# Kernel optimization log

Measured on AMD Instinct MI355X. Metric: run time of the kernel, lower is better.

The kernel has to match this reference:

```python
import jax, jax.numpy as jnp
import numpy as np

DIM, DK, DV = 1024, 128, 128

def setup_inputs() -> dict:
    key = jax.random.key(0)
    ks = jax.random.split(key, 7)
    X = jax.random.normal(ks[0], (4, 4096, DIM), dtype=jnp.float32)
    s = DIM ** -0.5
    Wq = jax.random.normal(ks[1], (DIM, DK), dtype=jnp.float32) * s
    bq = jnp.zeros((DK,), dtype=jnp.float32)
    Wk = jax.random.normal(ks[2], (DIM, DK), dtype=jnp.float32) * s
    bk = jnp.zeros((DK,), dtype=jnp.float32)
    Wv = jax.random.normal(ks[3], (DIM, DV), dtype=jnp.float32) * s
    bv = jnp.zeros((DV,), dtype=jnp.float32)
    return {"X": X, "Wq": Wq, "bq": bq, "Wk": Wk, "bk": bk, "Wv": Wv, "bv": bv}

def reference(X, Wq, bq, Wk, bk, Wv, bv):
    scale = DK ** -0.5
    q = X @ Wq + bq              # [B, S, dk]
    k = X @ Wk + bk              # [B, S, dk]
    v = X @ Wv + bv              # [B, S, dv]
    attn = jnp.einsum('bqd,bkd->bqk', q, k) * scale  # [B, S, S]
    attn = jax.nn.softmax(attn, axis=-1)
    return jnp.einsum('bqk,bkd->bqd', attn, v)       # [B, S, dv]
```

## Files before the change

### kernel.cpp

```cpp
#include <hip/hip_runtime.h>

#define NB 4
#define SEQ 4096
#define DIMK 1024
#define DKV 128
#define SCALE 0.08838834764831845f

typedef float  f32x4  __attribute__((ext_vector_type(4)));
typedef float  f32x16 __attribute__((ext_vector_type(16)));
typedef _Float16 f16x8 __attribute__((ext_vector_type(8)));

static __device__ __forceinline__ int pkrtz(float a, float b) {
    auto h = __builtin_amdgcn_cvt_pkrtz(a, b);
    return __builtin_bit_cast(int, h);
}

__global__ void prep_wt(const float* __restrict__ Wq, const float* __restrict__ Wk,
                        const float* __restrict__ Wv, _Float16* __restrict__ WT) {
    int tid = blockIdx.x * 256 + threadIdx.x;
    int n  = tid & 127;
    int k  = (tid >> 7) & 1023;
    int w3 = tid >> 17;
    const float* W = (w3 == 0) ? Wq : (w3 == 1) ? Wk : Wv;
    WT[((size_t)w3 * 128 + n) * 1024 + k] = (_Float16)W[(size_t)k * 128 + n];
}

__global__ __launch_bounds__(256, 2) void qkv_proj(
    const float* __restrict__ X,
    const float* __restrict__ bq, const float* __restrict__ bk, const float* __restrict__ bv,
    const _Float16* __restrict__ WT,
    _Float16* __restrict__ Qh, _Float16* __restrict__ Kh, _Float16* __restrict__ VTh) {

    __shared__ __attribute__((aligned(16))) char WTs[2][128 * 144];
    const int t = threadIdx.x;
    const int w = t >> 6, l = t & 63;
    const int lrow = l & 15, lg = l >> 4;
    const int w3   = blockIdx.x % 3;
    const int tile = blockIdx.x / 3;
    const int r0 = tile * 64;

    f32x4 acc[8] = {};
    const float* xrow = X + (size_t)(r0 + w * 16 + lrow) * DIMK;
    const _Float16* Wbase = WT + (size_t)w3 * 128 * 1024;

    const int srow = t >> 3, spart = t & 7;

    {
        int4 wreg[4];
        #pragma unroll
        for (int i = 0; i < 4; ++i)
            wreg[i] = *(const int4*)(Wbase + (size_t)(srow + 32 * i) * 1024 + spart * 8);
        #pragma unroll
        for (int i = 0; i < 4; ++i)
            *(int4*)(WTs[0] + (srow + 32 * i) * 144 + spart * 16) = wreg[i];
    }
    float4 xc0 = *(const float4*)(xrow + lg * 8);
    float4 xc1 = *(const float4*)(xrow + lg * 8 + 4);
    float4 xc2 = *(const float4*)(xrow + 32 + lg * 8);
    float4 xc3 = *(const float4*)(xrow + 32 + lg * 8 + 4);
    __syncthreads();

    for (int kt = 0; kt < 16; ++kt) {
        const int cur = kt & 1;
        const int k0n = ((kt + 1) & 15) * 64;
        float4 xn0 = *(const float4*)(xrow + k0n + lg * 8);
        float4 xn1 = *(const float4*)(xrow + k0n + lg * 8 + 4);
        float4 xn2 = *(const float4*)(xrow + k0n + 32 + lg * 8);
        float4 xn3 = *(const float4*)(xrow + k0n + 32 + lg * 8 + 4);
        int4 wreg[4];
        #pragma unroll
        for (int i = 0; i < 4; ++i)
            wreg[i] = *(const int4*)(Wbase + (size_t)(srow + 32 * i) * 1024 + k0n + spart * 8);

        #pragma unroll
        for (int kk = 0; kk < 2; ++kk) {
            f16x8 a;
            float4 u = kk ? xc2 : xc0, v = kk ? xc3 : xc1;
            a[0] = (_Float16)u.x; a[1] = (_Float16)u.y; a[2] = (_Float16)u.z; a[3] = (_Float16)u.w;
            a[4] = (_Float16)v.x; a[5] = (_Float16)v.y; a[6] = (_Float16)v.z; a[7] = (_Float16)v.w;
            #pragma unroll
            for (int n = 0; n < 8; ++n) {
                f16x8 bf = *(const f16x8*)(WTs[cur] + (n * 16 + lrow) * 144 +
                                           kk * 64 + lg * 16);
                acc[n] = __builtin_amdgcn_mfma_f32_16x16x32_f16(a, bf, acc[n], 0, 0, 0);
            }
        }
        #pragma unroll
        for (int i = 0; i < 4; ++i)
            *(int4*)(WTs[cur ^ 1] + (srow + 32 * i) * 144 + spart * 16) = wreg[i];
        __syncthreads();
        xc0 = xn0; xc1 = xn1; xc2 = xn2; xc3 = xn3;
    }

    const float* bias = (w3 == 0) ? bq : (w3 == 1) ? bk : bv;
    #pragma unroll
    for (int n = 0; n < 8; ++n) {
        int col = n * 16 + lrow;
        float bv_ = bias[col];
        #pragma unroll
        for (int j = 0; j < 4; ++j) {
            int grow = r0 + w * 16 + lg * 4 + j;
            float val = acc[n][j] + bv_;
            if (w3 == 0) {
                Qh[(size_t)grow * DKV + col] = (_Float16)(val * SCALE);
            } else if (w3 == 1) {
                Kh[(size_t)grow * DKV + col] = (_Float16)val;
            } else {
                int b = grow >> 12, sp = grow & 4095;
                VTh[((size_t)b * DKV + col) * SEQ + sp] = (_Float16)val;
            }
        }
    }
}

__global__ __launch_bounds__(256, 2) void attn_kernel(
    const _Float16* __restrict__ Qh, const _Float16* __restrict__ Kh,
    const _Float16* __restrict__ VTh, float* __restrict__ out) {

    __shared__ __attribute__((aligned(16))) char lds[65536];

    const int t = threadIdx.x;
    const int w = t >> 6, l = t & 63;
    const int lq = l & 31;
    const int hi = l >> 5;

    const int work = (blockIdx.x & 7) * 64 + (blockIdx.x >> 3);
    const int b  = work >> 7;
    const int qt = work & 127;
    const int q0 = qt * 32;

    char* Kw = lds + w * 16384;
    char* Vw = Kw + 8192;

    f16x8 qf[8];
    #pragma unroll
    for (int c = 0; c < 8; ++c)
        qf[c] = *(const f16x8*)(Qh + (size_t)(b * SEQ + q0 + lq) * DKV + c * 16 + hi * 8);

    f32x16 o[4] = {};
    float m = -INFINITY, lsum = 0.f;

    const _Float16* Kbase = Kh + (size_t)(b * SEQ + w * 1024) * DKV;
    const _Float16* Vbase = VTh + (size_t)b * DKV * SEQ + w * 1024;

    const int krow = l >> 4, kpart = l & 15;
    const int vdv  = l >> 2, vp = l & 3;

    {
        int4 kreg[8], vreg[8];
        #pragma unroll
        for (int i = 0; i < 8; ++i)
            kreg[i] = *(const int4*)(Kbase + (size_t)(krow + 4 * i) * DKV + kpart * 8);
        #pragma unroll
        for (int i = 0; i < 8; ++i)
            vreg[i] = *(const int4*)(Vbase + (size_t)(vdv + 16 * i) * SEQ + vp * 8);
        #pragma unroll
        for (int i = 0; i < 8; ++i) {
            int row = krow + 4 * i;
            *(int4*)(Kw + row * 256 + ((kpart * 16) ^ ((row & 15) << 4))) = kreg[i];
        }
        #pragma unroll
        for (int i = 0; i < 8; ++i) {
            int dv = vdv + 16 * i;
            *(int4*)(Vw + dv * 64 + ((vp ^ ((dv >> 1) & 3)) * 16)) = vreg[i];
        }
    }

    for (int kt = 0; kt < 32; ++kt) {
        const int kn = ((kt + 1) & 31) * 32;
        int4 kreg[8], vreg[8];
        #pragma unroll
        for (int i = 0; i < 8; ++i)
            kreg[i] = *(const int4*)(Kbase + (size_t)(kn + krow + 4 * i) * DKV + kpart * 8);
        #pragma unroll
        for (int i = 0; i < 8; ++i)
            vreg[i] = *(const int4*)(Vbase + (size_t)(vdv + 16 * i) * SEQ + kn + vp * 8);

        asm volatile("s_waitcnt lgkmcnt(0)" ::: "memory");
        __builtin_amdgcn_sched_barrier(0);

        f32x16 sa = {}, sb = {};
        #pragma unroll
        for (int c = 0; c < 4; ++c) {
            f16x8 kfa = *(const f16x8*)(Kw + lq * 256 +
                                        (((2 * c + hi) * 16) ^ ((lq & 15) << 4)));
            f16x8 kfb = *(const f16x8*)(Kw + lq * 256 +
                                        (((2 * (c + 4) + hi) * 16) ^ ((lq & 15) << 4)));
            sa = __builtin_amdgcn_mfma_f32_32x32x16_f16(kfa, qf[c], sa, 0, 0, 0);
            sb = __builtin_amdgcn_mfma_f32_32x32x16_f16(kfb, qf[c + 4], sb, 0, 0, 0);
        }
        f32x16 s = sa + sb;

        float red[8];
        #pragma unroll
        for (int r = 0; r < 8; ++r) red[r] = fmaxf(s[2 * r], s[2 * r + 1]);
        #pragma unroll
        for (int r = 0; r < 4; ++r) red[r] = fmaxf(red[r], red[r + 4]);
        red[0] = fmaxf(red[0], red[2]);
        red[1] = fmaxf(red[1], red[3]);
        float tm = fmaxf(red[0], red[1]);
        tm = fmaxf(tm, __shfl_xor(tm, 32));

        if (__any(tm > m + 8.f)) {
            float mnew = fmaxf(m, tm);
            float corr = __expf(m - mnew);
            m = mnew;
            lsum *= corr;
            #pragma unroll
            for (int dvt = 0; dvt < 4; ++dvt) o[dvt] *= corr;
        }
        #pragma unroll
        for (int r = 0; r < 16; ++r) s[r] = __expf(s[r] - m);
        float sr[8];
        #pragma unroll
        for (int r = 0; r < 8; ++r) sr[r] = s[2 * r] + s[2 * r + 1];
        #pragma unroll
        for (int r = 0; r < 4; ++r) sr[r] += sr[r + 4];
        sr[0] += sr[2]; sr[1] += sr[3];
        float ts = sr[0] + sr[1];
        ts += __shfl_xor(ts, 32);
        lsum += ts;

        int wv[8];
        #pragma unroll
        for (int i = 0; i < 8; ++i) wv[i] = pkrtz(s[2 * i], s[2 * i + 1]);

        #pragma unroll
        for (int s_ = 0; s_ < 2; ++s_) {
            const int base = s_ * 4;
            int x0 = __shfl_xor(wv[base + 0], 32);
            int x1 = __shfl_xor(wv[base + 1], 32);
            int x2 = __shfl_xor(wv[base + 2], 32);
            int x3 = __shfl_xor(wv[base + 3], 32);
            union { int i[4]; f16x8 v; } bu;
            bu.i[0] = hi ? x2 : wv[base + 0];
            bu.i[1] = hi ? x3 : wv[base + 1];
            bu.i[2] = hi ? wv[base + 2] : x0;
            bu.i[3] = hi ? wv[base + 3] : x1;
            #pragma unroll
            for (int dvt = 0; dvt < 4; ++dvt) {
                int rv = dvt * 32 + lq;
                f16x8 vf = *(const f16x8*)(Vw + rv * 64 +
                                           (((s_ * 2 + hi) ^ ((rv >> 1) & 3)) * 16));
                o[dvt] = __builtin_amdgcn_mfma_f32_32x32x16_f16(vf, bu.v, o[dvt], 0, 0, 0);
            }
        }

        #pragma unroll
        for (int i = 0; i < 8; ++i) {
            int row = krow + 4 * i;
            *(int4*)(Kw + row * 256 + ((kpart * 16) ^ ((row & 15) << 4))) = kreg[i];
        }
        #pragma unroll
        for (int i = 0; i < 8; ++i) {
            int dv = vdv + 16 * i;
            *(int4*)(Vw + dv * 64 + ((vp ^ ((dv >> 1) & 3)) * 16)) = vreg[i];
        }
    }

    float* obuf  = (float*)lds;
    float* mlbuf = (float*)(lds + 49152);

    __syncthreads();
    if (w == 1 || w == 3) {
        int sb_ = (w == 3);
        #pragma unroll
        for (int dvt = 0; dvt < 4; ++dvt)
            #pragma unroll
            for (int r = 0; r < 16; ++r)
                obuf[sb_ * 4096 + (dvt * 16 + r) * 64 + l] = o[dvt][r];
        if (l < 32) {
            mlbuf[sb_ * 64 + l * 2 + 0] = m;
            mlbuf[sb_ * 64 + l * 2 + 1] = lsum;
        }
    }
    __syncthreads();
    if (w == 0 || w == 2) {
        int sb_ = (w == 2);
        float mo  = mlbuf[sb_ * 64 + lq * 2 + 0];
        float lo_ = mlbuf[sb_ * 64 + lq * 2 + 1];
        float mn = fmaxf(m, mo);
        float ca = __expf(m - mn);
        float cb = __expf(mo - mn);
        m = mn;
        lsum = lsum * ca + lo_ * cb;
        #pragma unroll
        for (int dvt = 0; dvt < 4; ++dvt)
            #pragma unroll
            for (int r = 0; r < 16; ++r)
                o[dvt][r] = o[dvt][r] * ca + obuf[sb_ * 4096 + (dvt * 16 + r) * 64 + l] * cb;
    }
    __syncthreads();
    if (w == 2) {
        #pragma unroll
        for (int dvt = 0; dvt < 4; ++dvt)
            #pragma unroll
            for (int r = 0; r < 16; ++r)
                obuf[(dvt * 16 + r) * 64 + l] = o[dvt][r];
        if (l < 32) {
            mlbuf[l * 2 + 0] = m;
            mlbuf[l * 2 + 1] = lsum;
        }
    }
    __syncthreads();
    if (w == 0) {
        float mo  = mlbuf[lq * 2 + 0];
        float lo_ = mlbuf[lq * 2 + 1];
        float mn = fmaxf(m, mo);
        float ca = __expf(m - mn);
        float cb = __expf(mo - mn);
        float rl = 1.0f / (lsum * ca + lo_ * cb);
        #pragma unroll
        for (int dvt = 0; dvt < 4; ++dvt)
            #pragma unroll
            for (int r = 0; r < 16; ++r)
                o[dvt][r] = (o[dvt][r] * ca + obuf[(dvt * 16 + r) * 64 + l] * cb) * rl;
    }
    __syncthreads();
    float* tbuf = (float*)lds;
    if (w == 0) {
        #pragma unroll
        for (int dvt = 0; dvt < 4; ++dvt)
            #pragma unroll
            for (int r = 0; r < 16; ++r) {
                int dv = dvt * 32 + (r & 3) + 8 * (r >> 2) + 4 * hi;
                tbuf[lq * 132 + dv] = o[dvt][r];
            }
    }
    __syncthreads();
    const size_t obase = (size_t)(b * SEQ + qt * 32) * DKV;
    int row = t >> 3, c0 = (t & 7) * 16;
    #pragma unroll
    for (int i = 0; i < 4; ++i) {
        float4 v = *(const float4*)(tbuf + row * 132 + c0 + i * 4);
        *(float4*)(out + obase + row * 128 + c0 + i * 4) = v;
    }
}

extern "C" void kernel_launch(void* const* d_in, const int* in_sizes, int n_in,
                              void* d_out, int out_size, void* d_ws, size_t ws_size,
                              hipStream_t stream) {
    const float* X  = (const float*)d_in[0];
    const float* Wq = (const float*)d_in[1];
    const float* bq = (const float*)d_in[2];
    const float* Wk = (const float*)d_in[3];
    const float* bk = (const float*)d_in[4];
    const float* Wv = (const float*)d_in[5];
    const float* bv = (const float*)d_in[6];
    float* out = (float*)d_out;

    const size_t nqe = (size_t)NB * SEQ * DKV;
    _Float16* Qh  = (_Float16*)d_ws;
    _Float16* Kh  = Qh  + nqe;
    _Float16* VTh = Kh  + nqe;
    _Float16* WTh = VTh + nqe;

    prep_wt<<<(3 * 1024 * 128) / 256, 256, 0, stream>>>(Wq, Wk, Wv, WTh);
    qkv_proj<<<(NB * SEQ / 64) * 3, 256, 0, stream>>>(X, bq, bk, bv, WTh, Qh, Kh, VTh);
    attn_kernel<<<NB * 128, 256, 0, stream>>>(Qh, Kh, VTh, out);
}
```

Before: 119.9 us.

## Stage K/V tiles with direct global-to-LDS loads instead of register staging

Replaces the register-staged prefetch of K and V tiles (global load into VGPRs, then LDS store) with global_load_lds 16-byte transfers that write straight into LDS, with the swizzle moved to the global source address. K for the next tile is issued right after the QK MFMAs and V after the PV MFMAs, each guarded by an lgkmcnt wait. This frees the 16 int4 prefetch registers and removes the LDS store instructions. The trade-off is less latency hiding, since the next tile now loads into the same single buffer mid-iteration and the loop waits on vmcnt(0) at the top of every iteration.

```diff
diff --git a/kernel.cpp b/kernel.cpp
--- a/kernel.cpp
+++ b/kernel.cpp
@@ -13,6 +13,11 @@
 static __device__ __forceinline__ int pkrtz(float a, float b) {
     auto h = __builtin_amdgcn_cvt_pkrtz(a, b);
     return __builtin_bit_cast(int, h);
+}
+
+static __device__ __forceinline__ void gll16(const void* g, void* l) {
+    __builtin_amdgcn_global_load_lds((const __attribute__((address_space(1))) char*)g,
+                                     (__attribute__((address_space(3))) char*)l, 16, 0, 0);
 }
 
 __global__ void prep_wt(const float* __restrict__ Wq, const float* __restrict__ Wk,
@@ -143,40 +148,33 @@
     const _Float16* Kbase = Kh + (size_t)(b * SEQ + w * 1024) * DKV;
     const _Float16* Vbase = VTh + (size_t)b * DKV * SEQ + w * 1024;
 
-    const int krow = l >> 4, kpart = l & 15;
-    const int vdv  = l >> 2, vp = l & 3;
-
-    {
-        int4 kreg[8], vreg[8];
-        #pragma unroll
-        for (int i = 0; i < 8; ++i)
-            kreg[i] = *(const int4*)(Kbase + (size_t)(krow + 4 * i) * DKV + kpart * 8);
-        #pragma unroll
-        for (int i = 0; i < 8; ++i)
-            vreg[i] = *(const int4*)(Vbase + (size_t)(vdv + 16 * i) * SEQ + vp * 8);
-        #pragma unroll
-        for (int i = 0; i < 8; ++i) {
-            int row = krow + 4 * i;
-            *(int4*)(Kw + row * 256 + ((kpart * 16) ^ ((row & 15) << 4))) = kreg[i];
-        }
-        #pragma unroll
-        for (int i = 0; i < 8; ++i) {
-            int dv = vdv + 16 * i;
-            *(int4*)(Vw + dv * 64 + ((vp ^ ((dv >> 1) & 3)) * 16)) = vreg[i];
-        }
-    }
+    const int krow_ = l >> 4;
+    const int vdv_  = l >> 2;
+
+#define STAGE_K(KOFF) {                                                                   \
+        _Pragma("unroll")                                                                 \
+        for (int i = 0; i < 8; ++i) {                                                     \
+            int row = 4 * i + krow_;                                                      \
+            int part = (l & 15) ^ (row & 15);                                             \
+            gll16(Kbase + (size_t)((KOFF) + row) * DKV + part * 8, Kw + i * 1024);        \
+        }                                                                                 \
+    }
+#define STAGE_V(KOFF) {                                                                   \
+        _Pragma("unroll")                                                                 \
+        for (int i = 0; i < 8; ++i) {                                                     \
+            int dv = 16 * i + vdv_;                                                       \
+            int p = (l & 3) ^ ((dv >> 1) & 3);                                            \
+            gll16(Vbase + (size_t)dv * SEQ + (KOFF) + p * 8, Vw + i * 1024);              \
+        }                                                                                 \
+    }
+
+    STAGE_K(0)
+    STAGE_V(0)
 
     for (int kt = 0; kt < 32; ++kt) {
         const int kn = ((kt + 1) & 31) * 32;
-        int4 kreg[8], vreg[8];
-        #pragma unroll
-        for (int i = 0; i < 8; ++i)
-            kreg[i] = *(const int4*)(Kbase + (size_t)(kn + krow + 4 * i) * DKV + kpart * 8);
-        #pragma unroll
-        for (int i = 0; i < 8; ++i)
-            vreg[i] = *(const int4*)(Vbase + (size_t)(vdv + 16 * i) * SEQ + kn + vp * 8);
-
-        asm volatile("s_waitcnt lgkmcnt(0)" ::: "memory");
+
+        asm volatile("s_waitcnt vmcnt(0)" ::: "memory");
         __builtin_amdgcn_sched_barrier(0);
 
         f32x16 sa = {}, sb = {};
@@ -190,6 +188,10 @@
             sb = __builtin_amdgcn_mfma_f32_32x32x16_f16(kfb, qf[c + 4], sb, 0, 0, 0);
         }
         f32x16 s = sa + sb;
+
+        asm volatile("s_waitcnt lgkmcnt(0)" ::: "memory");
+        __builtin_amdgcn_sched_barrier(0);
+        STAGE_K(kn)
 
         float red[8];
         #pragma unroll
@@ -246,17 +248,12 @@
             }
         }
 
-        #pragma unroll
-        for (int i = 0; i < 8; ++i) {
-            int row = krow + 4 * i;
-            *(int4*)(Kw + row * 256 + ((kpart * 16) ^ ((row & 15) << 4))) = kreg[i];
-        }
-        #pragma unroll
-        for (int i = 0; i < 8; ++i) {
-            int dv = vdv + 16 * i;
-            *(int4*)(Vw + dv * 64 + ((vp ^ ((dv >> 1) & 3)) * 16)) = vreg[i];
-        }
-    }
+        asm volatile("s_waitcnt lgkmcnt(0)" ::: "memory");
+        __builtin_amdgcn_sched_barrier(0);
+        STAGE_V(kn)
+    }
+#undef STAGE_K
+#undef STAGE_V
 
     float* obuf  = (float*)lds;
     float* mlbuf = (float*)(lds + 49152);
```

After: 118.9 us. No clear change (-0.9%).
